# Optimization experiments

Hardware: AMD Instinct MI355X
Metric: run time of the kernel (lower is better)

The kernel has to match this reference:

```python
import jax, jax.numpy as jnp
import numpy as np

B, N, M = 4, 8192, 8192


def setup_inputs() -> dict:
    key = jax.random.key(0)
    k1, k2 = jax.random.split(key)
    xyz1 = jax.random.normal(k1, (B, N, 3), dtype=jnp.float32)
    xyz2 = jax.random.normal(k2, (B, M, 3), dtype=jnp.float32)
    return {"xyz1": xyz1, "xyz2": xyz2}


def _chamfer(xyz1, xyz2):
    # Squared Euclidean pairwise distances via the expansion
    # ||a-b||^2 = ||a||^2 + ||b||^2 - 2 a.b  (avoids a [B,N,M,3] diff tensor).
    sq1 = jnp.sum(xyz1 * xyz1, axis=-1)              # [B,N]
    sq2 = jnp.sum(xyz2 * xyz2, axis=-1)              # [B,M]
    inner = jnp.einsum('bnd,bmd->bnm', xyz1, xyz2)   # [B,N,M]
    d = sq1[:, :, None] + sq2[:, None, :] - 2.0 * inner
    d = jnp.maximum(d, 0.0)
    dist1 = jnp.min(d, axis=2)  # [B,N] nearest xyz2 point for each xyz1 point
    dist2 = jnp.min(d, axis=1)  # [B,M] nearest xyz1 point for each xyz2 point
    return dist1, dist2


def reference(xyz1, xyz2):
    return _chamfer(xyz1, xyz2)
```

## Files before the change

### kernel.cpp

```cpp
#include <hip/hip_runtime.h>


#define TPB   256
#define QPT   8
#define QPB   (TPB * QPT)
#define SEG   16
#define NPTS  8192
#define NB    4
#define RTILE (NPTS / SEG)

__global__ void chamfer_init_out(unsigned int* __restrict__ out, int n) {
    int i = blockIdx.x * blockDim.x + threadIdx.x;
    if (i < n) out[i] = 0x7F800000u;
}

__global__ __launch_bounds__(TPB, 2) void chamfer_kernel(
    const float* __restrict__ xyz1,
    const float* __restrict__ xyz2,
    unsigned int* __restrict__ out)
{
    __shared__ float4 tile[RTILE];

    int bid = blockIdx.x;
    int s   = bid & (SEG - 1); bid >>= 4;
    int qt  = bid & 3;         bid >>= 2;
    int b   = bid & 3;         bid >>= 2;
    int dir = bid;

    const float* qptr = dir ? xyz2 : xyz1;
    const float* rptr = dir ? xyz1 : xyz2;
    const int outbase = dir * (NB * NPTS) + b * NPTS;

    for (int j = threadIdx.x; j < RTILE; j += TPB) {
        int g = (b * NPTS + s * RTILE + j) * 3;
        float x = rptr[g], y = rptr[g + 1], z = rptr[g + 2];
        tile[j] = make_float4(x, y, z, x * x + y * y + z * z);
    }

    float qx2[QPT], qy2[QPT], qz2[QPT], qs[QPT], m[QPT];
#pragma unroll
    for (int k = 0; k < QPT; ++k) {
        int q = qt * QPB + k * TPB + threadIdx.x;
        int g = (b * NPTS + q) * 3;
        float x = qptr[g], y = qptr[g + 1], z = qptr[g + 2];
        qx2[k] = -2.0f * x;
        qy2[k] = -2.0f * y;
        qz2[k] = -2.0f * z;
        qs[k]  = x * x + y * y + z * z;
        m[k]   = INFINITY;
    }
    __syncthreads();

    for (int j = 0; j < RTILE; j += 4) {
        float4 r0 = tile[j + 0];
        float4 r1 = tile[j + 1];
        float4 r2 = tile[j + 2];
        float4 r3 = tile[j + 3];
#pragma unroll
        for (int k = 0; k < QPT; ++k) {
            float d0 = fmaf(qz2[k], r0.z, fmaf(qy2[k], r0.y, fmaf(qx2[k], r0.x, r0.w)));
            float d1 = fmaf(qz2[k], r1.z, fmaf(qy2[k], r1.y, fmaf(qx2[k], r1.x, r1.w)));
            float d2 = fmaf(qz2[k], r2.z, fmaf(qy2[k], r2.y, fmaf(qx2[k], r2.x, r2.w)));
            float d3 = fmaf(qz2[k], r3.z, fmaf(qy2[k], r3.y, fmaf(qx2[k], r3.x, r3.w)));
            m[k] = fminf(m[k], fminf(fminf(d0, d1), fminf(d2, d3)));
        }
    }

#pragma unroll
    for (int k = 0; k < QPT; ++k) {
        int q = qt * QPB + k * TPB + threadIdx.x;
        float d = fmaxf(qs[k] + m[k], 0.0f);
        atomicMin(&out[outbase + q], __float_as_uint(d));
    }
}

extern "C" void kernel_launch(void* const* d_in, const int* in_sizes, int n_in,
                              void* d_out, int out_size, void* d_ws, size_t ws_size,
                              hipStream_t stream) {
    const float* xyz1 = (const float*)d_in[0];
    const float* xyz2 = (const float*)d_in[1];
    unsigned int* out = (unsigned int*)d_out;

    hipLaunchKernelGGL(chamfer_init_out,
                       dim3((out_size + TPB - 1) / TPB), dim3(TPB), 0, stream,
                       out, out_size);

    hipLaunchKernelGGL(chamfer_kernel,
                       dim3(2 * NB * (NPTS / QPB) * SEG), dim3(TPB), 0, stream,
                       xyz1, xyz2, out);
}
```

Baseline: 95.59 us.

## Use packed FP32 FMA with paired SoA tile layout and min3 reductions

```diff
diff --git a/kernel.cpp b/kernel.cpp
--- a/kernel.cpp
+++ b/kernel.cpp
@@ -1,28 +1,43 @@
 #include <hip/hip_runtime.h>
 
 
-#define TPB   256
-#define QPT   8
-#define QPB   (TPB * QPT)
-#define SEG   16
-#define NPTS  8192
-#define NB    4
-#define RTILE (NPTS / SEG)
+typedef float f32x2 __attribute__((ext_vector_type(2)));
+
+#define TPB    256
+#define QPT    8
+#define QPB    (TPB * QPT)
+#define SEG    32
+#define NPTS   8192
+#define NB     4
+#define RTILE  (NPTS / SEG)
+#define RPAIRS (RTILE / 2)
+
+__device__ __forceinline__ f32x2 pk_fma(f32x2 a, f32x2 b, f32x2 c) {
+    f32x2 d;
+    asm("v_pk_fma_f32 %0, %1, %2, %3" : "=v"(d) : "v"(a), "v"(b), "v"(c));
+    return d;
+}
+
+__device__ __forceinline__ float min3f(float a, float b, float c) {
+    float d;
+    asm("v_min3_f32 %0, %1, %2, %3" : "=v"(d) : "v"(a), "v"(b), "v"(c));
+    return d;
+}
 
 __global__ void chamfer_init_out(unsigned int* __restrict__ out, int n) {
     int i = blockIdx.x * blockDim.x + threadIdx.x;
     if (i < n) out[i] = 0x7F800000u;
 }
 
-__global__ __launch_bounds__(TPB, 2) void chamfer_kernel(
+__global__ __launch_bounds__(TPB, 4) void chamfer_kernel(
     const float* __restrict__ xyz1,
     const float* __restrict__ xyz2,
     unsigned int* __restrict__ out)
 {
-    __shared__ float4 tile[RTILE];
+    __shared__ float4 tile[2 * RPAIRS];
 
     int bid = blockIdx.x;
-    int s   = bid & (SEG - 1); bid >>= 4;
+    int s   = bid & (SEG - 1); bid >>= 5;
     int qt  = bid & 3;         bid >>= 2;
     int b   = bid & 3;         bid >>= 2;
     int dir = bid;
@@ -31,38 +46,49 @@
     const float* rptr = dir ? xyz1 : xyz2;
     const int outbase = dir * (NB * NPTS) + b * NPTS;
 
-    for (int j = threadIdx.x; j < RTILE; j += TPB) {
-        int g = (b * NPTS + s * RTILE + j) * 3;
-        float x = rptr[g], y = rptr[g + 1], z = rptr[g + 2];
-        tile[j] = make_float4(x, y, z, x * x + y * y + z * z);
+    for (int p = threadIdx.x; p < RPAIRS; p += TPB) {
+        int g = (b * NPTS + s * RTILE + 2 * p) * 3;
+        float x0 = rptr[g + 0], y0 = rptr[g + 1], z0 = rptr[g + 2];
+        float x1 = rptr[g + 3], y1 = rptr[g + 4], z1 = rptr[g + 5];
+        tile[2 * p + 0] = make_float4(x0, x1, y0, y1);
+        tile[2 * p + 1] = make_float4(z0, z1,
+                                      x0 * x0 + y0 * y0 + z0 * z0,
+                                      x1 * x1 + y1 * y1 + z1 * z1);
     }
 
-    float qx2[QPT], qy2[QPT], qz2[QPT], qs[QPT], m[QPT];
+    f32x2 qx[QPT], qy[QPT], qz[QPT];
+    float qs[QPT], m[QPT];
 #pragma unroll
     for (int k = 0; k < QPT; ++k) {
         int q = qt * QPB + k * TPB + threadIdx.x;
         int g = (b * NPTS + q) * 3;
         float x = qptr[g], y = qptr[g + 1], z = qptr[g + 2];
-        qx2[k] = -2.0f * x;
-        qy2[k] = -2.0f * y;
-        qz2[k] = -2.0f * z;
-        qs[k]  = x * x + y * y + z * z;
-        m[k]   = INFINITY;
+        qx[k].x = qx[k].y = -2.0f * x;
+        qy[k].x = qy[k].y = -2.0f * y;
+        qz[k].x = qz[k].y = -2.0f * z;
+        qs[k] = x * x + y * y + z * z;
+        m[k]  = INFINITY;
     }
     __syncthreads();
 
-    for (int j = 0; j < RTILE; j += 4) {
-        float4 r0 = tile[j + 0];
-        float4 r1 = tile[j + 1];
-        float4 r2 = tile[j + 2];
-        float4 r3 = tile[j + 3];
+    for (int p = 0; p < 2 * RPAIRS; p += 4) {
+        float4 u0 = tile[p + 0];
+        float4 v0 = tile[p + 1];
+        float4 u1 = tile[p + 2];
+        float4 v1 = tile[p + 3];
+        f32x2 x01; x01.x = u0.x; x01.y = u0.y;
+        f32x2 y01; y01.x = u0.z; y01.y = u0.w;
+        f32x2 z01; z01.x = v0.x; z01.y = v0.y;
+        f32x2 w01; w01.x = v0.z; w01.y = v0.w;
+        f32x2 x23; x23.x = u1.x; x23.y = u1.y;
+        f32x2 y23; y23.x = u1.z; y23.y = u1.w;
+        f32x2 z23; z23.x = v1.x; z23.y = v1.y;
+        f32x2 w23; w23.x = v1.z; w23.y = v1.w;
 #pragma unroll
         for (int k = 0; k < QPT; ++k) {
-            float d0 = fmaf(qz2[k], r0.z, fmaf(qy2[k], r0.y, fmaf(qx2[k], r0.x, r0.w)));
-            float d1 = fmaf(qz2[k], r1.z, fmaf(qy2[k], r1.y, fmaf(qx2[k], r1.x, r1.w)));
-            float d2 = fmaf(qz2[k], r2.z, fmaf(qy2[k], r2.y, fmaf(qx2[k], r2.x, r2.w)));
-            float d3 = fmaf(qz2[k], r3.z, fmaf(qy2[k], r3.y, fmaf(qx2[k], r3.x, r3.w)));
-            m[k] = fminf(m[k], fminf(fminf(d0, d1), fminf(d2, d3)));
+            f32x2 d01 = pk_fma(qz[k], z01, pk_fma(qy[k], y01, pk_fma(qx[k], x01, w01)));
+            f32x2 d23 = pk_fma(qz[k], z23, pk_fma(qy[k], y23, pk_fma(qx[k], x23, w23)));
+            m[k] = min3f(min3f(d01.x, d01.y, d23.x), d23.y, m[k]);
         }
     }
 
```

New measurement: 94.98 us. About the same (-0.6%).

## Compute chamfer distances on MFMA using split-bf16 augmented vectors

Applied to the files above, without the earlier changes.

```diff
diff --git a/kernel.cpp b/kernel.cpp
--- a/kernel.cpp
+++ b/kernel.cpp
@@ -1,76 +1,137 @@
 #include <hip/hip_runtime.h>
 
 
-#define TPB   256
-#define QPT   8
-#define QPB   (TPB * QPT)
-#define SEG   16
-#define NPTS  8192
-#define NB    4
-#define RTILE (NPTS / SEG)
+typedef __bf16 bf16_t;
+typedef __bf16 bf16x8 __attribute__((ext_vector_type(8)));
+typedef float  f32x16 __attribute__((ext_vector_type(16)));
+
+#define NPTS    8192
+#define NB      4
+#define NSETPTS (NB * NPTS)
+#define TPB     256
+#define WAVES   4
+#define QPW     2
+#define QC      (WAVES * QPW * 32)
+#define SEGR    4
+#define RC      (NPTS / SEGR)
+#define RT      (RC / 32)
 
 __global__ void chamfer_init_out(unsigned int* __restrict__ out, int n) {
     int i = blockIdx.x * blockDim.x + threadIdx.x;
     if (i < n) out[i] = 0x7F800000u;
 }
 
-__global__ __launch_bounds__(TPB, 2) void chamfer_kernel(
-    const float* __restrict__ xyz1,
-    const float* __restrict__ xyz2,
+__device__ __forceinline__ void split2(float v, bf16_t& h, bf16_t& l) {
+    h = (bf16_t)v;
+    l = (bf16_t)(v - (float)h);
+}
+
+__global__ void chamfer_prep(const float* __restrict__ xyz1,
+                             const float* __restrict__ xyz2,
+                             bf16_t* __restrict__ a16,
+                             bf16_t* __restrict__ b16) {
+    int i = blockIdx.x * blockDim.x + threadIdx.x;
+    const float* src = (i >= NSETPTS) ? xyz2 : xyz1;
+    int p = i & (NSETPTS - 1);
+    float x = src[3 * p], y = src[3 * p + 1], z = src[3 * p + 2];
+    float sq = x * x + y * y + z * z;
+
+    bf16_t m2xh, m2xl, m2yh, m2yl, m2zh, m2zl;
+    split2(-2.f * x, m2xh, m2xl);
+    split2(-2.f * y, m2yh, m2yl);
+    split2(-2.f * z, m2zh, m2zl);
+    bf16_t xh, xl, yh, yl, zh, zl;
+    split2(x, xh, xl); split2(y, yh, yl); split2(z, zh, zl);
+    bf16_t sqh, sql;
+    split2(sq, sqh, sql);
+    bf16_t one = (bf16_t)1.0f, zero = (bf16_t)0.0f;
+
+    bf16_t A[16]  = { m2xh, m2yh, m2zh,  m2xl, m2yl, m2zl,
+                      m2xh, m2yh, m2zh,  sqh, sql, one, one, zero, zero, zero };
+    bf16_t Bv[16] = { xh, yh, zh,  xh, yh, zh,  xl, yl, zl,
+                      one, one, sqh, sql, zero, zero, zero };
+
+    const int perm[16] = {0,1,2,3, 8,9,10,11, 4,5,6,7, 12,13,14,15};
+    bf16_t* ao = a16 + (size_t)i * 16;
+    bf16_t* bo = b16 + (size_t)i * 16;
+#pragma unroll
+    for (int j = 0; j < 16; ++j) { ao[j] = A[perm[j]]; bo[j] = Bv[perm[j]]; }
+}
+
+__global__ __launch_bounds__(TPB, 4) void chamfer_main(
+    const bf16_t* __restrict__ a16,
+    const bf16_t* __restrict__ b16,
     unsigned int* __restrict__ out)
 {
-    __shared__ float4 tile[RTILE];
+    __shared__ float red[WAVES][QPW][32][33];
 
     int bid = blockIdx.x;
-    int s   = bid & (SEG - 1); bid >>= 4;
-    int qt  = bid & 3;         bid >>= 2;
-    int b   = bid & 3;         bid >>= 2;
+    int s   = bid & (SEGR - 1); bid >>= 2;
+    int qp  = bid & 31;         bid >>= 5;
+    int b   = bid & 3;          bid >>= 2;
     int dir = bid;
 
-    const float* qptr = dir ? xyz2 : xyz1;
-    const float* rptr = dir ? xyz1 : xyz2;
-    const int outbase = dir * (NB * NPTS) + b * NPTS;
+    int wave = threadIdx.x >> 6;
+    int lane = threadIdx.x & 63;
+    int col  = lane & 31;
+    int h    = lane >> 5;
 
-    for (int j = threadIdx.x; j < RTILE; j += TPB) {
-        int g = (b * NPTS + s * RTILE + j) * 3;
-        float x = rptr[g], y = rptr[g + 1], z = rptr[g + 2];
-        tile[j] = make_float4(x, y, z, x * x + y * y + z * z);
+    const bf16_t* ap = a16 + ((size_t)dir * NB + b) * NPTS * 16;
+    const bf16_t* bp = b16 + ((size_t)(1 - dir) * NB + b) * NPTS * 16;
+
+    int qbase = qp * QC + wave * (QPW * 32);
+    const bf16x8* a0p = (const bf16x8*)(ap + (size_t)(qbase + col) * 16) + h;
+    const bf16x8* a1p = (const bf16x8*)(ap + (size_t)(qbase + 32 + col) * 16) + h;
+    bf16x8 af0 = *a0p;
+    bf16x8 af1 = *a1p;
+
+    int rbase = s * RC;
+    const bf16x8* bptr = (const bf16x8*)(bp + (size_t)(rbase + col) * 16) + h;
+
+    f32x16 rm0, rm1, zacc;
+#pragma unroll
+    for (int g = 0; g < 16; ++g) { rm0[g] = INFINITY; rm1[g] = INFINITY; zacc[g] = 0.f; }
+
+    bf16x8 bf = bptr[0];
+#pragma unroll 2
+    for (int t = 0; t < RT; ++t) {
+        int tn = (t + 1 < RT) ? (t + 1) : t;
+        bf16x8 bnx = bptr[(size_t)tn * 64];
+        f32x16 acc0 = __builtin_amdgcn_mfma_f32_32x32x16_bf16(af0, bf, zacc, 0, 0, 0);
+        f32x16 acc1 = __builtin_amdgcn_mfma_f32_32x32x16_bf16(af1, bf, zacc, 0, 0, 0);
+#pragma unroll
+        for (int g = 0; g < 16; ++g) rm0[g] = fminf(rm0[g], acc0[g]);
+#pragma unroll
+        for (int g = 0; g < 16; ++g) rm1[g] = fminf(rm1[g], acc1[g]);
+        bf = bnx;
     }
 
-    float qx2[QPT], qy2[QPT], qz2[QPT], qs[QPT], m[QPT];
 #pragma unroll
-    for (int k = 0; k < QPT; ++k) {
-        int q = qt * QPB + k * TPB + threadIdx.x;
-        int g = (b * NPTS + q) * 3;
-        float x = qptr[g], y = qptr[g + 1], z = qptr[g + 2];
-        qx2[k] = -2.0f * x;
-        qy2[k] = -2.0f * y;
-        qz2[k] = -2.0f * z;
-        qs[k]  = x * x + y * y + z * z;
-        m[k]   = INFINITY;
+    for (int g = 0; g < 16; ++g) {
+        int row = (g & 3) + 8 * (g >> 2) + 4 * h;
+        red[wave][0][row][col] = rm0[g];
+        red[wave][1][row][col] = rm1[g];
     }
     __syncthreads();
 
-    for (int j = 0; j < RTILE; j += 4) {
-        float4 r0 = tile[j + 0];
-        float4 r1 = tile[j + 1];
-        float4 r2 = tile[j + 2];
-        float4 r3 = tile[j + 3];
+    {
+        int w  = threadIdx.x >> 6;
+        int rem = threadIdx.x & 63;
+        int qt = rem >> 5;
+        int r  = rem & 31;
+        const float* rowp = &red[w][qt][r][0];
+        float v0 = rowp[0], v1 = rowp[1], v2 = rowp[2], v3 = rowp[3];
 #pragma unroll
-        for (int k = 0; k < QPT; ++k) {
-            float d0 = fmaf(qz2[k], r0.z, fmaf(qy2[k], r0.y, fmaf(qx2[k], r0.x, r0.w)));
-            float d1 = fmaf(qz2[k], r1.z, fmaf(qy2[k], r1.y, fmaf(qx2[k], r1.x, r1.w)));
-            float d2 = fmaf(qz2[k], r2.z, fmaf(qy2[k], r2.y, fmaf(qx2[k], r2.x, r2.w)));
-            float d3 = fmaf(qz2[k], r3.z, fmaf(qy2[k], r3.y, fmaf(qx2[k], r3.x, r3.w)));
-            m[k] = fminf(m[k], fminf(fminf(d0, d1), fminf(d2, d3)));
+        for (int c = 4; c < 32; c += 4) {
+            v0 = fminf(v0, rowp[c + 0]);
+            v1 = fminf(v1, rowp[c + 1]);
+            v2 = fminf(v2, rowp[c + 2]);
+            v3 = fminf(v3, rowp[c + 3]);
         }
-    }
-
-#pragma unroll
-    for (int k = 0; k < QPT; ++k) {
-        int q = qt * QPB + k * TPB + threadIdx.x;
-        float d = fmaxf(qs[k] + m[k], 0.0f);
-        atomicMin(&out[outbase + q], __float_as_uint(d));
+        float v = fminf(fminf(v0, v1), fminf(v2, v3));
+        v = fmaxf(v, 0.f);
+        unsigned idx = (unsigned)(dir * NSETPTS + b * NPTS + qp * QC + threadIdx.x);
+        atomicMin(&out[idx], __float_as_uint(v));
     }
 }
 
@@ -81,11 +142,18 @@
     const float* xyz2 = (const float*)d_in[1];
     unsigned int* out = (unsigned int*)d_out;
 
+    bf16_t* a16 = (bf16_t*)d_ws;
+    bf16_t* b16 = a16 + (size_t)2 * NSETPTS * 16;
+
     hipLaunchKernelGGL(chamfer_init_out,
                        dim3((out_size + TPB - 1) / TPB), dim3(TPB), 0, stream,
                        out, out_size);
 
-    hipLaunchKernelGGL(chamfer_kernel,
-                       dim3(2 * NB * (NPTS / QPB) * SEG), dim3(TPB), 0, stream,
-                       xyz1, xyz2, out);
+    hipLaunchKernelGGL(chamfer_prep,
+                       dim3(2 * NSETPTS / TPB), dim3(TPB), 0, stream,
+                       xyz1, xyz2, a16, b16);
+
+    hipLaunchKernelGGL(chamfer_main,
+                       dim3(2 * NB * (NPTS / QC) * SEGR), dim3(TPB), 0, stream,
+                       a16, b16, out);
 }
```

Result: faster. 80.19 us (-16.1%).
